# Kernel optimization log

Measured on AMD Instinct MI355X. Metric: run time of the kernel, lower is better.

## Reference

```python
import jax, jax.numpy as jnp
import numpy as np

EMB_DIM = 1024
HEAD_DIM = 64


def setup_inputs() -> dict:
    key = jax.random.key(0)
    kx, kq, kk, kv = jax.random.split(key, 4)
    B, S = 4, 4096
    x = jax.random.normal(kx, (B, S, EMB_DIM), dtype=jnp.float32)
    # nn.Linear weights are [out, in]; kaiming-uniform-ish init scale
    lim = 1.0 / np.sqrt(EMB_DIM)
    Wq = jax.random.uniform(kq, (HEAD_DIM, EMB_DIM), jnp.float32, -lim, lim)
    Wk = jax.random.uniform(kk, (HEAD_DIM, EMB_DIM), jnp.float32, -lim, lim)
    Wv = jax.random.uniform(kv, (HEAD_DIM, EMB_DIM), jnp.float32, -lim, lim)
    return {"x": x, "Wq": Wq, "Wk": Wk, "Wv": Wv}


def reference(x, Wq, Wk, Wv):
    # x: [B, S, E]; W*: [H, E] (torch Linear layout) -> project with x @ W.T
    Q = jnp.einsum("bse,he->bsh", x, Wq)
    K = jnp.einsum("bse,he->bsh", x, Wk)
    V = jnp.einsum("bse,he->bsh", x, Wv)
    # NOTE: source scales by emb_dim**0.5, not head_dim**0.5 — keep faithful.
    scores = jnp.einsum("bqh,bkh->bqk", Q, K) / jnp.sqrt(jnp.float32(x.shape[-1]))
    S = scores.shape[-1]
    causal = jnp.tril(jnp.ones((S, S), dtype=bool))  # [S, S]
    scores = jnp.where(causal, scores, -jnp.inf)
    attn = jax.nn.softmax(scores, axis=-1)
    return jnp.einsum("bqk,bkh->bqh", attn, V)
```

## Files before the change

kernel.cpp:

```cpp
#include <hip/hip_runtime.h>
#include <hip/hip_bf16.h>
#include <math.h>

#define B_ 4
#define S_ 4096
#define E_ 1024

typedef __attribute__((ext_vector_type(8))) short bf16x8;
typedef __attribute__((ext_vector_type(4))) short bf16x4;
typedef __attribute__((ext_vector_type(4))) float f32x4;

__device__ __forceinline__ unsigned short f2bf(float f) {
  unsigned u = __float_as_uint(f);
  u = u + 0x7fffu + ((u >> 16) & 1u);
  return (unsigned short)(u >> 16);
}

__global__ __launch_bounds__(256) void proj_kernel(
    const float* __restrict__ x, const float* __restrict__ Wq,
    const float* __restrict__ Wk, const float* __restrict__ Wv,
    unsigned short* __restrict__ Qp, unsigned short* __restrict__ Kb,
    unsigned short* __restrict__ Vt)
{
  __shared__ __align__(16) unsigned short xs[64*64];
  __shared__ __align__(16) unsigned short wl[192*64];
  const int tid = threadIdx.x;
  const int wave = tid >> 6, lane = tid & 63;
  const int l15 = lane & 15, l4 = lane >> 4;
  const int m0 = blockIdx.x * 64;

  f32x4 acc[12];
  #pragma unroll
  for (int i = 0; i < 12; i++) acc[i] = (f32x4)0.f;

  f32x4 xr[4], wr[12];
  #pragma unroll
  for (int i = 0; i < 4; i++) {
    int c = tid + i*256; int row = c >> 4, cc = c & 15;
    xr[i] = *(const f32x4*)(x + (size_t)(m0 + row)*E_ + cc*4);
  }
  #pragma unroll
  for (int i = 0; i < 12; i++) {
    int c = tid + i*256; int n = c >> 4, cc = c & 15;
    const float* Wsrc = (n < 64) ? (Wq + (size_t)n*E_)
                     : ((n < 128) ? (Wk + (size_t)(n-64)*E_)
                                  : (Wv + (size_t)(n-128)*E_));
    wr[i] = *(const f32x4*)(Wsrc + cc*4);
  }

  for (int ks = 0; ks < 16; ks++) {
    __syncthreads();
    #pragma unroll
    for (int i = 0; i < 4; i++) {
      int c = tid + i*256; int row = c >> 4, cc = c & 15;
      bf16x4 v;
      v[0] = (short)f2bf(xr[i][0]); v[1] = (short)f2bf(xr[i][1]);
      v[2] = (short)f2bf(xr[i][2]); v[3] = (short)f2bf(xr[i][3]);
      *(bf16x4*)((char*)xs + row*128 + ((cc*8) ^ ((row&7)<<4))) = v;
    }
    #pragma unroll
    for (int i = 0; i < 12; i++) {
      int c = tid + i*256; int n = c >> 4, cc = c & 15;
      bf16x4 v;
      v[0] = (short)f2bf(wr[i][0]); v[1] = (short)f2bf(wr[i][1]);
      v[2] = (short)f2bf(wr[i][2]); v[3] = (short)f2bf(wr[i][3]);
      *(bf16x4*)((char*)wl + n*128 + ((cc*8) ^ ((n&7)<<4))) = v;
    }
    if (ks < 15) {
      #pragma unroll
      for (int i = 0; i < 4; i++) {
        int c = tid + i*256; int row = c >> 4, cc = c & 15;
        xr[i] = *(const f32x4*)(x + (size_t)(m0 + row)*E_ + (ks+1)*64 + cc*4);
      }
      #pragma unroll
      for (int i = 0; i < 12; i++) {
        int c = tid + i*256; int n = c >> 4, cc = c & 15;
        const float* Wsrc = (n < 64) ? (Wq + (size_t)n*E_)
                         : ((n < 128) ? (Wk + (size_t)(n-64)*E_)
                                      : (Wv + (size_t)(n-128)*E_));
        wr[i] = *(const f32x4*)(Wsrc + (ks+1)*64 + cc*4);
      }
    }
    __syncthreads();
    const int arow = wave*16 + l15;
    const int aswz = (arow&7)<<4;
    bf16x8 a0 = *(const bf16x8*)((const char*)xs + arow*128 + ((l4*16) ^ aswz));
    bf16x8 a1 = *(const bf16x8*)((const char*)xs + arow*128 + ((64 + l4*16) ^ aswz));
    #pragma unroll
    for (int ntl = 0; ntl < 12; ntl++) {
      int brow = ntl*16 + l15;
      int bswz = (brow&7)<<4;
      bf16x8 b0 = *(const bf16x8*)((const char*)wl + brow*128 + ((l4*16) ^ bswz));
      bf16x8 b1 = *(const bf16x8*)((const char*)wl + brow*128 + ((64 + l4*16) ^ bswz));
      acc[ntl] = __builtin_amdgcn_mfma_f32_16x16x32_bf16(a0, b0, acc[ntl], 0, 0, 0);
      acc[ntl] = __builtin_amdgcn_mfma_f32_16x16x32_bf16(a1, b1, acc[ntl], 0, 0, 0);
    }
  }

  const float QSC = 0.04508422f;
  const int mb = m0 + wave*16 + l4*4;
  #pragma unroll
  for (int ntl = 0; ntl < 4; ntl++) {
    int col = ntl*16 + l15;
    #pragma unroll
    for (int r = 0; r < 4; r++)
      Qp[(size_t)(mb + r)*64 + col] = f2bf(acc[ntl][r] * QSC);
  }
  #pragma unroll
  for (int ntl = 0; ntl < 4; ntl++) {
    int col = ntl*16 + l15;
    #pragma unroll
    for (int r = 0; r < 4; r++)
      Kb[(size_t)(mb + r)*64 + col] = f2bf(acc[4+ntl][r]);
  }
  const int b = m0 >> 12;
  const int sb = (m0 & 4095) + wave*16 + l4*4;
  #pragma unroll
  for (int ntl = 0; ntl < 4; ntl++) {
    int d = ntl*16 + l15;
    bf16x4 v;
    #pragma unroll
    for (int r = 0; r < 4; r++) v[r] = (short)f2bf(acc[8+ntl][r]);
    *(bf16x4*)(Vt + (size_t)(b*64 + d)*S_ + sb) = v;
  }
}

__global__ __launch_bounds__(256) void attn_kernel(
    const unsigned short* __restrict__ Qp,
    const unsigned short* __restrict__ Kb,
    const unsigned short* __restrict__ Vt,
    float* __restrict__ out)
{
  __shared__ __align__(16) unsigned short Ks[64*64];
  __shared__ __align__(16) unsigned short Vs[64*64];
  __shared__ __align__(16) float mergeO[4][16][64];
  __shared__ float mstats[4][16][2];

  const int tid = threadIdx.x;
  const int wave = tid >> 6, lane = tid & 63;
  const int l15 = lane & 15, l4 = lane >> 4;
  const int g = wave >> 1, h = wave & 1;
  const int b = blockIdx.x >> 6;
  const int p = blockIdx.x & 63;

  const unsigned short* Qb  = Qp + (size_t)b*S_*64;
  const unsigned short* Kbb = Kb + (size_t)b*S_*64;
  const unsigned short* Vtb = Vt + (size_t)b*64*S_;
  float* outb = out + (size_t)b*S_*64;

  #pragma unroll 1
  for (int half = 0; half < 2; half++) {
    const int jq = half ? (127 - p) : p;
    const int q0 = jq * 32;
    const int ntile = (jq >> 1) + 1;
    const int qrow = q0 + g*16 + l15;

    bf16x8 qf0 = *(const bf16x8*)(Qb + (size_t)qrow*64 + l4*8);
    bf16x8 qf1 = *(const bf16x8*)(Qb + (size_t)qrow*64 + 32 + l4*8);

    float m = -INFINITY, lsum = 0.f;
    f32x4 acc[4];
    #pragma unroll
    for (int i = 0; i < 4; i++) acc[i] = (f32x4)0.f;

    f32x4 kreg[2], vreg[2];
    #pragma unroll
    for (int i = 0; i < 2; i++) {
      int c = tid + i*256; int row = c >> 3, cc = c & 7;
      kreg[i] = *(const f32x4*)((const char*)Kbb + (size_t)row*128 + cc*16);
      vreg[i] = *(const f32x4*)((const char*)Vtb + (size_t)row*8192 + cc*16);
    }

    for (int t = 0; t < ntile; t++) {
      __syncthreads();
      #pragma unroll
      for (int i = 0; i < 2; i++) {
        int c = tid + i*256; int row = c >> 3, cc = c & 7;
        *(f32x4*)((char*)Ks + row*128 + ((cc*16) ^ ((row&7)<<4))) = kreg[i];
        *(f32x4*)((char*)Vs + row*128 + ((cc*16) ^ ((row&7)<<4))) = vreg[i];
      }
      if (t + 1 < ntile) {
        int k0 = (t+1)*64;
        #pragma unroll
        for (int i = 0; i < 2; i++) {
          int c = tid + i*256; int row = c >> 3, cc = c & 7;
          kreg[i] = *(const f32x4*)((const char*)Kbb + (size_t)(k0+row)*128 + cc*16);
          vreg[i] = *(const f32x4*)((const char*)Vtb + (size_t)row*8192 + (size_t)k0*2 + cc*16);
        }
      }
      __syncthreads();

      f32x4 sv[2];
      #pragma unroll
      for (int st = 0; st < 2; st++) {
        int krow = (2*h + st)*16 + l15;
        const char* kbp = (const char*)Ks + krow*128;
        int swz = (krow&7)<<4;
        bf16x8 k0f = *(const bf16x8*)(kbp + ((l4*16) ^ swz));
        bf16x8 k1f = *(const bf16x8*)(kbp + ((64 + l4*16) ^ swz));
        f32x4 z = (f32x4)0.f;
        z = __builtin_amdgcn_mfma_f32_16x16x32_bf16(k0f, qf0, z, 0, 0, 0);
        z = __builtin_amdgcn_mfma_f32_16x16x32_bf16(k1f, qf1, z, 0, 0, 0);
        sv[st] = z;
      }
      if (t == ntile - 1) {
        #pragma unroll
        for (int st = 0; st < 2; st++) {
          #pragma unroll
          for (int r = 0; r < 4; r++) {
            int kg = t*64 + (2*h + st)*16 + l4*4 + r;
            if (kg > qrow) sv[st][r] = -INFINITY;
          }
        }
      }
      float pmax = sv[0][0];
      #pragma unroll
      for (int st = 0; st < 2; st++) {
        #pragma unroll
        for (int r = 0; r < 4; r++) pmax = fmaxf(pmax, sv[st][r]);
      }
      pmax = fmaxf(pmax, __shfl_xor(pmax, 16, 64));
      pmax = fmaxf(pmax, __shfl_xor(pmax, 32, 64));
      float mnew = fmaxf(m, pmax);
      float msafe = (mnew == -INFINITY) ? 0.f : mnew;
      float scale = exp2f(m - msafe);
      float pv[8]; float psum = 0.f;
      #pragma unroll
      for (int i = 0; i < 8; i++) {
        pv[i] = exp2f(sv[i>>2][i&3] - msafe);
        psum += pv[i];
      }
      psum += __shfl_xor(psum, 16, 64);
      psum += __shfl_xor(psum, 32, 64);
      lsum = lsum*scale + psum;
      m = mnew;
      #pragma unroll
      for (int i = 0; i < 4; i++) acc[i] *= scale;
      bf16x8 pf;
      #pragma unroll
      for (int i = 0; i < 8; i++) pf[i] = (short)f2bf(pv[i]);
      #pragma unroll
      for (int dt = 0; dt < 4; dt++) {
        int drow = dt*16 + l15;
        const char* vb = (const char*)Vs + drow*128;
        int swz = (drow&7)<<4;
        bf16x4 v0 = *(const bf16x4*)(vb + ((h*64 + l4*8) ^ swz));
        bf16x4 v1 = *(const bf16x4*)(vb + ((h*64 + 32 + l4*8) ^ swz));
        bf16x8 vf;
        #pragma unroll
        for (int i = 0; i < 4; i++) { vf[i] = v0[i]; vf[i+4] = v1[i]; }
        acc[dt] = __builtin_amdgcn_mfma_f32_16x16x32_bf16(vf, pf, acc[dt], 0, 0, 0);
      }
    }

    __syncthreads();
    #pragma unroll
    for (int dt = 0; dt < 4; dt++)
      *(f32x4*)&mergeO[wave][l15][dt*16 + l4*4] = acc[dt];
    if (lane < 16) { mstats[wave][lane][0] = m; mstats[wave][lane][1] = lsum; }
    __syncthreads();
    {
      int ql = tid >> 3, dc = tid & 7;
      int gg = ql >> 4, q16 = ql & 15;
      float m1 = mstats[gg*2+0][q16][0], s1 = mstats[gg*2+0][q16][1];
      float m2 = mstats[gg*2+1][q16][0], s2 = mstats[gg*2+1][q16][1];
      float m12 = fmaxf(m1, m2);
      float a1 = exp2f(m1 - m12), a2 = exp2f(m2 - m12);
      float inv = 1.f / (s1*a1 + s2*a2);
      a1 *= inv; a2 *= inv;
      #pragma unroll
      for (int i = 0; i < 2; i++) {
        int d = dc*8 + i*4;
        f32x4 o1 = *(const f32x4*)&mergeO[gg*2+0][q16][d];
        f32x4 o2 = *(const f32x4*)&mergeO[gg*2+1][q16][d];
        f32x4 o = o1*a1 + o2*a2;
        *(f32x4*)(outb + (size_t)(q0 + ql)*64 + d) = o;
      }
    }
  }
}

extern "C" void kernel_launch(void* const* d_in, const int* in_sizes, int n_in,
                              void* d_out, int out_size, void* d_ws, size_t ws_size,
                              hipStream_t stream)
{
  const float* x  = (const float*)d_in[0];
  const float* Wq = (const float*)d_in[1];
  const float* Wk = (const float*)d_in[2];
  const float* Wv = (const float*)d_in[3];
  unsigned short* Qp  = (unsigned short*)d_ws;
  unsigned short* Kbp = Qp  + (size_t)B_*S_*64;
  unsigned short* Vtp = Kbp + (size_t)B_*S_*64;
  float* out = (float*)d_out;

  hipLaunchKernelGGL(proj_kernel, dim3(256), dim3(256), 0, stream,
                     x, Wq, Wk, Wv, Qp, Kbp, Vtp);
  hipLaunchKernelGGL(attn_kernel, dim3(256), dim3(256), 0, stream,
                     Qp, Kbp, Vtp, out);
}
```

Baseline: 165.6 us.

## Split attention KV range across blocks and merge partials in a separate kernel

Adds split-K (flash-decoding style) parallelism: each query tile's causal key range is divided across NS blocks, and NS is chosen from the available workspace size. Each block writes unnormalized partial outputs plus max/sum stats, and a new merge kernel combines them with log-sum-exp rescaling. This raises the grid from 256 blocks so more of the many CUs on MI355X are occupied. The cost is partial-result traffic to global memory and an extra kernel launch. The merge LDS buffer is also padded to reduce bank conflicts.

```diff
diff --git a/kernel.cpp b/kernel.cpp
--- a/kernel.cpp
+++ b/kernel.cpp
@@ -129,19 +129,24 @@
     const unsigned short* __restrict__ Qp,
     const unsigned short* __restrict__ Kb,
     const unsigned short* __restrict__ Vt,
-    float* __restrict__ out)
+    float* __restrict__ out,
+    float* __restrict__ Opart, float* __restrict__ spart, int NS)
 {
   __shared__ __align__(16) unsigned short Ks[64*64];
   __shared__ __align__(16) unsigned short Vs[64*64];
-  __shared__ __align__(16) float mergeO[4][16][64];
+  __shared__ __align__(16) float mergeO[4][16][68];
   __shared__ float mstats[4][16][2];
 
   const int tid = threadIdx.x;
   const int wave = tid >> 6, lane = tid & 63;
   const int l15 = lane & 15, l4 = lane >> 4;
   const int g = wave >> 1, h = wave & 1;
-  const int b = blockIdx.x >> 6;
-  const int p = blockIdx.x & 63;
+
+  const int bid = blockIdx.x;
+  const int lg = (NS == 4) ? 2 : ((NS == 2) ? 1 : 0);
+  const int b  = (bid >> 1) & 3;
+  const int ks = (bid >> 3) & (NS - 1);
+  const int p  = ((bid >> (3 + lg)) << 1) | (bid & 1);
 
   const unsigned short* Qb  = Qp + (size_t)b*S_*64;
   const unsigned short* Kbb = Kb + (size_t)b*S_*64;
@@ -153,6 +158,9 @@
     const int jq = half ? (127 - p) : p;
     const int q0 = jq * 32;
     const int ntile = (jq >> 1) + 1;
+    const int tb = ntile / NS, tr = ntile % NS;
+    const int kbeg = ks*tb + (ks < tr ? ks : tr);
+    const int kend = kbeg + tb + (ks < tr ? 1 : 0);
     const int qrow = q0 + g*16 + l15;
 
     bf16x8 qf0 = *(const bf16x8*)(Qb + (size_t)qrow*64 + l4*8);
@@ -164,14 +172,16 @@
     for (int i = 0; i < 4; i++) acc[i] = (f32x4)0.f;
 
     f32x4 kreg[2], vreg[2];
-    #pragma unroll
-    for (int i = 0; i < 2; i++) {
-      int c = tid + i*256; int row = c >> 3, cc = c & 7;
-      kreg[i] = *(const f32x4*)((const char*)Kbb + (size_t)row*128 + cc*16);
-      vreg[i] = *(const f32x4*)((const char*)Vtb + (size_t)row*8192 + cc*16);
-    }
-
-    for (int t = 0; t < ntile; t++) {
+    if (kbeg < kend) {
+      #pragma unroll
+      for (int i = 0; i < 2; i++) {
+        int c = tid + i*256; int row = c >> 3, cc = c & 7;
+        kreg[i] = *(const f32x4*)((const char*)Kbb + (size_t)(kbeg*64 + row)*128 + cc*16);
+        vreg[i] = *(const f32x4*)((const char*)Vtb + (size_t)row*8192 + (size_t)kbeg*128 + cc*16);
+      }
+    }
+
+    for (int t = kbeg; t < kend; t++) {
       __syncthreads();
       #pragma unroll
       for (int i = 0; i < 2; i++) {
@@ -179,7 +189,7 @@
         *(f32x4*)((char*)Ks + row*128 + ((cc*16) ^ ((row&7)<<4))) = kreg[i];
         *(f32x4*)((char*)Vs + row*128 + ((cc*16) ^ ((row&7)<<4))) = vreg[i];
       }
-      if (t + 1 < ntile) {
+      if (t + 1 < kend) {
         int k0 = (t+1)*64;
         #pragma unroll
         for (int i = 0; i < 2; i++) {
@@ -265,19 +275,67 @@
       float m1 = mstats[gg*2+0][q16][0], s1 = mstats[gg*2+0][q16][1];
       float m2 = mstats[gg*2+1][q16][0], s2 = mstats[gg*2+1][q16][1];
       float m12 = fmaxf(m1, m2);
-      float a1 = exp2f(m1 - m12), a2 = exp2f(m2 - m12);
-      float inv = 1.f / (s1*a1 + s2*a2);
-      a1 *= inv; a2 *= inv;
-      #pragma unroll
-      for (int i = 0; i < 2; i++) {
-        int d = dc*8 + i*4;
-        f32x4 o1 = *(const f32x4*)&mergeO[gg*2+0][q16][d];
-        f32x4 o2 = *(const f32x4*)&mergeO[gg*2+1][q16][d];
-        f32x4 o = o1*a1 + o2*a2;
-        *(f32x4*)(outb + (size_t)(q0 + ql)*64 + d) = o;
-      }
-    }
-  }
+      float msafe12 = (m12 == -INFINITY) ? 0.f : m12;
+      float a1 = exp2f(m1 - msafe12), a2 = exp2f(m2 - msafe12);
+      float s12 = s1*a1 + s2*a2;
+      if (NS == 1) {
+        float inv = 1.f / s12;
+        float b1 = a1*inv, b2 = a2*inv;
+        #pragma unroll
+        for (int i = 0; i < 2; i++) {
+          int d = dc*8 + i*4;
+          f32x4 o1 = *(const f32x4*)&mergeO[gg*2+0][q16][d];
+          f32x4 o2 = *(const f32x4*)&mergeO[gg*2+1][q16][d];
+          f32x4 o = o1*b1 + o2*b2;
+          *(f32x4*)(outb + (size_t)(q0 + ql)*64 + d) = o;
+        }
+      } else {
+        int slot = ((b*128 + jq)*NS + ks);
+        #pragma unroll
+        for (int i = 0; i < 2; i++) {
+          int d = dc*8 + i*4;
+          f32x4 o1 = *(const f32x4*)&mergeO[gg*2+0][q16][d];
+          f32x4 o2 = *(const f32x4*)&mergeO[gg*2+1][q16][d];
+          f32x4 o = o1*a1 + o2*a2;
+          *(f32x4*)(Opart + (size_t)slot*2048 + ql*64 + d) = o;
+        }
+        if (dc == 0) {
+          spart[(size_t)slot*64 + ql*2]     = m12;
+          spart[(size_t)slot*64 + ql*2 + 1] = s12;
+        }
+      }
+    }
+  }
+}
+
+__global__ __launch_bounds__(256) void merge_kernel(
+    const float* __restrict__ Opart, const float* __restrict__ spart,
+    float* __restrict__ out, int NS)
+{
+  const int bid = blockIdx.x;
+  const int b = bid >> 7, jq = bid & 127;
+  const int q0 = jq * 32;
+  const int ql = threadIdx.x >> 3, dc = threadIdx.x & 7;
+  const int base = (b*128 + jq) * NS;
+
+  float M = -INFINITY;
+  for (int i = 0; i < NS; i++)
+    M = fmaxf(M, spart[(size_t)(base+i)*64 + ql*2]);
+  float wsum = 0.f;
+  f32x4 o0 = (f32x4)0.f, o1 = (f32x4)0.f;
+  for (int i = 0; i < NS; i++) {
+    float mi = spart[(size_t)(base+i)*64 + ql*2];
+    float li = spart[(size_t)(base+i)*64 + ql*2 + 1];
+    float a = exp2f(mi - M);
+    wsum += li * a;
+    const float* op = Opart + (size_t)(base+i)*2048 + ql*64 + dc*8;
+    o0 += a * (*(const f32x4*)op);
+    o1 += a * (*(const f32x4*)(op + 4));
+  }
+  float inv = 1.f / wsum;
+  float* dst = out + (size_t)b*S_*64 + (size_t)(q0 + ql)*64 + dc*8;
+  *(f32x4*)dst = o0 * inv;
+  *(f32x4*)(dst + 4) = o1 * inv;
 }
 
 extern "C" void kernel_launch(void* const* d_in, const int* in_sizes, int n_in,
@@ -293,8 +351,18 @@
   unsigned short* Vtp = Kbp + (size_t)B_*S_*64;
   float* out = (float*)d_out;
 
+  const size_t qkv = (size_t)B_*S_*64*2*3;
+  const size_t per_ns = (size_t)512*2048*4 + (size_t)512*64*4;
+  int NS = (ws_size >= qkv + 4*per_ns) ? 4
+         : (ws_size >= qkv + 2*per_ns) ? 2 : 1;
+  float* Opart = (float*)((char*)d_ws + qkv);
+  float* spart = (float*)((char*)d_ws + qkv + (size_t)NS*512*2048*4);
+
   hipLaunchKernelGGL(proj_kernel, dim3(256), dim3(256), 0, stream,
                      x, Wq, Wk, Wv, Qp, Kbp, Vtp);
-  hipLaunchKernelGGL(attn_kernel, dim3(256), dim3(256), 0, stream,
-                     Qp, Kbp, Vtp, out);
-}
+  hipLaunchKernelGGL(attn_kernel, dim3(256*NS), dim3(256), 0, stream,
+                     Qp, Kbp, Vtp, out, Opart, spart, NS);
+  if (NS > 1)
+    hipLaunchKernelGGL(merge_kernel, dim3(512), dim3(256), 0, stream,
+                       Opart, spart, out, NS);
+}
```

After: 160.7 us. -3.0%, faster.
